# Kernel optimization log

Measured on AMD Instinct MI355X. Metric: run time of the kernel, lower is better.

## Reference

```python
import jax, jax.numpy as jnp
import numpy as np
from jax import lax

B, L_IN, DEC_LEN = 1024, 2048, 64
H = 128            # hidden_size
CARD, EMB = 200, 16  # categorical feature cardinality / embedding dim
VDIM = 4
IN_SIZE = EMB + 1 + 1  # cat-embed + continuous feat (Linear(1,1)) + target value


def setup_inputs() -> dict:
    key = jax.random.key(0)
    k = jax.random.split(key, 19)
    s = 1.0 / np.sqrt(H)  # torch LSTM/Linear default init scale
    u = lambda kk, shape: jax.random.uniform(kk, shape, minval=-s, maxval=s, dtype=jnp.float32)
    return {
        "cat_in": jax.random.randint(k[0], (B, L_IN), 0, CARD, dtype=jnp.int32),
        "cont_in": jax.random.normal(k[1], (B, L_IN, 1), dtype=jnp.float32),
        "X_in": jax.random.normal(k[2], (B, L_IN, 1), dtype=jnp.float32),
        "cat_out": jax.random.randint(k[3], (B, DEC_LEN), 0, CARD, dtype=jnp.int32),
        "cont_out": jax.random.normal(k[4], (B, DEC_LEN, 1), dtype=jnp.float32),
        # learned params
        "emb_table": jax.random.normal(k[5], (CARD, EMB), dtype=jnp.float32) * 0.02,
        "cont_w": jax.random.normal(k[6], (1, 1), dtype=jnp.float32) * 0.5,  # Linear(1,1,bias=False)
        "Wih_e": u(k[7], (4 * H, IN_SIZE)),
        "Whh_e": u(k[8], (4 * H, H)),
        "b_e": u(k[9], (4 * H,)),   # b_ih + b_hh folded together
        "Wih_d": u(k[10], (4 * H, IN_SIZE)),
        "Whh_d": u(k[11], (4 * H, H)),
        "b_d": u(k[12], (4 * H,)),
        "Wm": u(k[13], (1, H)), "bm": u(k[14], (1,)),
        "Ws": u(k[15], (1, H)), "bs": u(k[16], (1,)),
        "Wv": u(k[17], (VDIM, H)), "bv": u(k[18], (VDIM,)),
    }


def _lstm_cell(x, h, c, Wih, Whh, b):
    # torch gate order: i, f, g, o
    gates = x @ Wih.T + h @ Whh.T + b  # [B, 4H]
    i, f, g, o = jnp.split(gates, 4, axis=-1)
    c_new = jax.nn.sigmoid(f) * c + jax.nn.sigmoid(i) * jnp.tanh(g)
    h_new = jax.nn.sigmoid(o) * jnp.tanh(c_new)
    return h_new, c_new


def reference(cat_in, cont_in, X_in, cat_out, cont_out, emb_table, cont_w,
              Wih_e, Whh_e, b_e, Wih_d, Whh_d, b_d, Wm, bm, Ws, bs, Wv, bv):
    w00 = cont_w[0, 0]
    # feature embedding: Embedding for categorical, Linear(1,1,no bias) for continuous
    feats_in_embed = jnp.concatenate([emb_table[cat_in], cont_in * w00], axis=-1)  # [B,L,EMB+1]
    enc_in = jnp.concatenate([feats_in_embed, X_in], axis=-1)                      # [B,L,IN_SIZE]

    h0 = jnp.zeros((X_in.shape[0], H), dtype=X_in.dtype)

    def enc_step(carry, xt):
        h, c = carry
        return _lstm_cell(xt, h, c, Wih_e, Whh_e, b_e), None

    # encoder outputs are unused downstream; only the final (h, c) state matters
    (h, c), _ = lax.scan(enc_step, (h0, h0), jnp.swapaxes(enc_in, 0, 1))

    feats_out_embed = jnp.concatenate([emb_table[cat_out], cont_out * w00], axis=-1)  # [B,D,EMB+1]

    def dec_step(carry, feats_next):
        h, c, x_prev, f_prev = carry
        xt = jnp.concatenate([f_prev, x_prev], axis=-1)  # [B, IN_SIZE]
        h, c = _lstm_cell(xt, h, c, Wih_d, Whh_d, b_d)
        mu = h @ Wm.T + bm                     # [B,1]
        std = jax.nn.softplus(h @ Ws.T + bs)   # [B,1]
        v = h @ Wv.T + bv                      # [B,VDIM]
        return (h, c, mu, feats_next), (mu, std, v)

    init = (h, c, X_in[:, -1, :], feats_in_embed[:, -1, :])
    _, (means, stds, vs) = lax.scan(dec_step, init, jnp.swapaxes(feats_out_embed, 0, 1))
    # [D,B,*] -> [B,D,*]
    return (jnp.swapaxes(means, 0, 1), jnp.swapaxes(stds, 0, 1), jnp.swapaxes(vs, 0, 1))
```

## Files before the change

### kernel.cpp

```cpp
#include <hip/hip_runtime.h>
#include <math.h>

typedef _Float16 half8 __attribute__((ext_vector_type(8)));
typedef float float4v __attribute__((ext_vector_type(4)));

constexpr int Lc   = 2048;
constexpr int DECc = 64;
constexpr int Hc   = 128;
constexpr int EMBc = 16;
constexpr int INc  = 18;
constexpr int NBc  = 4;
constexpr int NTc  = 512;
constexpr int CARD = 200;
constexpr int ZS   = 160;


__device__ __forceinline__ float rcp_(float x) { return __builtin_amdgcn_rcpf(x); }
__device__ __forceinline__ float sigm(float x) { return rcp_(1.0f + __expf(-x)); }
__device__ __forceinline__ float tanh_(float x) { return 2.0f * rcp_(1.0f + __expf(-2.0f * x)) - 1.0f; }
__device__ __forceinline__ float softplus_(float x) { return __logf(1.0f + __expf(x)); }

__device__ __forceinline__ float sel4(float4v v, int q) {
    const float a = (q & 1) ? v[1] : v[0];
    const float b = (q & 1) ? v[3] : v[2];
    return (q & 2) ? b : a;
}

__global__ __launch_bounds__(NTc, 1) void rnnar_kernel(
    const int*   __restrict__ cat_in,  const float* __restrict__ cont_in,
    const float* __restrict__ X_in,    const int*   __restrict__ cat_out,
    const float* __restrict__ cont_out,const float* __restrict__ emb_table,
    const float* __restrict__ cont_w,
    const float* __restrict__ Wih_e, const float* __restrict__ Whh_e, const float* __restrict__ b_e,
    const float* __restrict__ Wih_d, const float* __restrict__ Whh_d, const float* __restrict__ b_d,
    const float* __restrict__ Wm, const float* __restrict__ bm,
    const float* __restrict__ Ws, const float* __restrict__ bs,
    const float* __restrict__ Wv, const float* __restrict__ bv,
    float* __restrict__ out)
{
    __shared__ _Float16      z_lds[2][NBc * ZS];
    __shared__ _Float16      emb_lds[CARD * EMBc];
    __shared__ _Float16      xo4[DECc * NBc];
    __shared__ unsigned char catob4[DECc * NBc];
    __shared__ float         h32_lds[NBc * 132];
    __shared__ float         wh_lds[6 * Hc];
    __shared__ float         hb_lds[8];
    __shared__ float         mu_lds[4];
    __shared__ float4v       x_lds[8][4][4][16];

    const int tid  = threadIdx.x;
    const int lane = tid & 63;
    const int wv   = tid >> 6;
    const int q    = lane >> 4;
    const int col  = lane & 15;
    const int cell = 16 * wv + col;
    const int bx   = col & 3;
    const int gu   = col >> 2;
    const int gb   = col & 3;
    const int b0   = blockIdx.x * NBc;
    const float w00 = cont_w[0];

    {
        int* z32 = (int*)&z_lds[0][0];
        for (int i = tid; i < NBc * ZS; i += NTc) z32[i] = 0;
    }
    for (int i = tid; i < CARD * EMBc; i += NTc) emb_lds[i] = (_Float16)emb_table[i];
    if (tid < NBc * DECc) {
        const int t = tid >> 2, b = tid & 3;
        catob4[tid] = (unsigned char)cat_out[(b0 + b) * DECc + t];
        xo4[tid]    = (_Float16)(cont_out[(b0 + b) * DECc + t] * w00);
    }
    for (int i = tid; i < 6 * Hc; i += NTc) {
        const int o = i >> 7, k = i & 127;
        wh_lds[i] = (o == 0) ? Wm[k] : (o == 1) ? Ws[k] : Wv[(o - 2) * Hc + k];
    }
    if (tid == 0) { hb_lds[0] = bm[0]; hb_lds[1] = bs[0]; }
    if (tid < 4)  { hb_lds[2 + tid] = bv[tid]; mu_lds[tid] = 0.0f; }

    half8 Bf[4][5];
    float bias_s[4];
    float w17_s[4];
    #define LOAD_T(WIH, WHH, BB)                                               \
    {                                                                          \
        _Pragma("unroll")                                                      \
        for (int gt = 0; gt < 4; ++gt) {                                       \
            const int row = gt * Hc + cell;                                    \
            _Pragma("unroll")                                                  \
            for (int kt = 0; kt < 5; ++kt) {                                   \
                half8 f;                                                       \
                _Pragma("unroll")                                              \
                for (int j = 0; j < 8; ++j) {                                  \
                    const int k = 32 * kt + 8 * q + j;                         \
                    float v = 0.0f;                                            \
                    if (k < Hc)             v = WHH[row * Hc + k];             \
                    else if (k < Hc + INc)  v = WIH[row * INc + (k - Hc)];     \
                    f[j] = (_Float16)v;                                        \
                }                                                              \
                Bf[gt][kt] = f;                                                \
            }                                                                  \
            bias_s[gt] = BB[row];                                              \
            w17_s[gt]  = WIH[row * INc + 17];                                  \
        }                                                                      \
    }

    #define BUILD_X(GCAT, GCONT, GX)                                           \
    {                                                                          \
        half8 ax;                                                              \
        _Pragma("unroll") for (int j = 0; j < 8; ++j) ax[j] = (_Float16)0.0f;  \
        if (q < 2)       ax = *(const half8*)&emb_lds[(GCAT) * EMBc + 8 * q];  \
        else if (q == 2) { ax[0] = (_Float16)((GCONT) * w00); ax[1] = (_Float16)(GX); } \
        _Pragma("unroll")                                                      \
        for (int gt = 0; gt < 4; ++gt) {                                       \
            float4v a = {bias_s[gt], bias_s[gt], bias_s[gt], bias_s[gt]};      \
            a = __builtin_amdgcn_mfma_f32_16x16x32_f16(ax, Bf[gt][4], a, 0, 0, 0); \
            x_lds[wv][q][gt][col] = a;                                         \
        }                                                                      \
    }

    LOAD_T(Wih_e, Whh_e, b_e);
    __syncthreads();

    int   g_cat;  float g_cont, g_X;
    {
        const long idx = (long)(b0 + gb) * Lc + gu;
        g_cat  = cat_in[idx];
        g_cont = cont_in[idx];
        g_X    = X_in[idx];
    }
    BUILD_X(g_cat, g_cont, g_X);

    float4v xinit[4];
    #pragma unroll
    for (int gt = 0; gt < 4; ++gt) xinit[gt] = x_lds[wv][0][gt][col];

    int p = 0;
    float c_reg = 0.f;

    for (int t = 0; t < Lc; ++t) {
        const _Float16* zr = &z_lds[p][0];
        _Float16*       zw = &z_lds[p ^ 1][0];

        const _Float16* ap = zr + bx * ZS + 8 * q;
        half8 Az[4];
        #pragma unroll
        for (int kt = 0; kt < 4; ++kt) Az[kt] = *(const half8*)(ap + 32 * kt);

        float4v acc[4];
        #pragma unroll
        for (int gt = 0; gt < 4; ++gt) {
            float4v a = xinit[gt];
            #pragma unroll
            for (int kt = 0; kt < 4; ++kt)
                a = __builtin_amdgcn_mfma_f32_16x16x32_f16(Az[kt], Bf[gt][kt], a, 0, 0, 0);
            acc[gt] = a;
        }

        if ((t & 3) == 2 && t + 2 < Lc) {
            const long idx = (long)(b0 + gb) * Lc + (t + 2 + gu);
            g_cat  = cat_in[idx];
            g_cont = cont_in[idx];
            g_X    = X_in[idx];
        }
        if ((t & 3) == 3 && t + 1 < Lc) BUILD_X(g_cat, g_cont, g_X);

        {
            const int sn = (t + 1) & 3;
            #pragma unroll
            for (int gt = 0; gt < 4; ++gt) xinit[gt] = x_lds[wv][sn][gt][col];
        }

        const float gi = sel4(acc[0], q);
        const float gf = sel4(acc[1], q);
        const float gg = sel4(acc[2], q);
        const float go = sel4(acc[3], q);

        const float cn = sigm(gf) * c_reg + sigm(gi) * tanh_(gg);
        c_reg = cn;
        zw[q * ZS + cell] = (_Float16)(sigm(go) * tanh_(cn));

        __syncthreads();
        p ^= 1;
    }

    LOAD_T(Wih_d, Whh_d, b_d);
    const float bm0 = hb_lds[0], bs0 = hb_lds[1];

    float4v acc_pre[4];
    {
        const long idx = (long)(b0 + bx) * Lc + (Lc - 1);
        const int   c0 = cat_in[idx];
        const float cc = cont_in[idx];
        const float xx = X_in[idx];
        half8 ax;
        #pragma unroll
        for (int j = 0; j < 8; ++j) ax[j] = (_Float16)0.0f;
        if (q < 2)       ax = *(const half8*)&emb_lds[c0 * EMBc + 8 * q];
        else if (q == 2) { ax[0] = (_Float16)(cc * w00); ax[1] = (_Float16)xx; }
        #pragma unroll
        for (int gt = 0; gt < 4; ++gt) {
            float4v a = {bias_s[gt], bias_s[gt], bias_s[gt], bias_s[gt]};
            acc_pre[gt] = __builtin_amdgcn_mfma_f32_16x16x32_f16(ax, Bf[gt][4], a, 0, 0, 0);
        }
    }
    __syncthreads();

    for (int t = 0; t < DECc; ++t) {
        const _Float16* zr = &z_lds[p][0];
        _Float16*       zw = &z_lds[p ^ 1][0];

        const float muq = mu_lds[q];

        const _Float16* ap = zr + bx * ZS + 8 * q;
        half8 Az[4];
        #pragma unroll
        for (int kt = 0; kt < 4; ++kt) Az[kt] = *(const half8*)(ap + 32 * kt);

        float4v acc[4];
        #pragma unroll
        for (int gt = 0; gt < 4; ++gt) {
            float4v a = acc_pre[gt];
            #pragma unroll
            for (int kt = 0; kt < 4; ++kt)
                a = __builtin_amdgcn_mfma_f32_16x16x32_f16(Az[kt], Bf[gt][kt], a, 0, 0, 0);
            acc[gt] = a;
        }

        {
            half8 ax;
            #pragma unroll
            for (int j = 0; j < 8; ++j) ax[j] = (_Float16)0.0f;
            if (q < 2)       ax = *(const half8*)&emb_lds[(int)catob4[t * 4 + bx] * EMBc + 8 * q];
            else if (q == 2) ax[0] = xo4[t * 4 + bx];
            #pragma unroll
            for (int gt = 0; gt < 4; ++gt) {
                float4v a = {bias_s[gt], bias_s[gt], bias_s[gt], bias_s[gt]};
                acc_pre[gt] = __builtin_amdgcn_mfma_f32_16x16x32_f16(ax, Bf[gt][4], a, 0, 0, 0);
            }
        }

        const float gi = sel4(acc[0], q) + muq * w17_s[0];
        const float gf = sel4(acc[1], q) + muq * w17_s[1];
        const float gg = sel4(acc[2], q) + muq * w17_s[2];
        const float go = sel4(acc[3], q) + muq * w17_s[3];

        const float cn = sigm(gf) * c_reg + sigm(gi) * tanh_(gg);
        c_reg = cn;
        const float hv = sigm(go) * tanh_(cn);
        zw[q * ZS + cell] = (_Float16)hv;
        h32_lds[q * 132 + cell] = hv;

        __syncthreads();

        if (tid < 384) {
            const int grp = tid >> 4;
            const int l16 = tid & 15;
            const int b   = grp & 3, o = grp >> 2;
            float s = 0.0f;
            #pragma unroll
            for (int j = 0; j < 8; ++j) {
                const int k = l16 + 16 * j;
                s += wh_lds[o * Hc + k] * h32_lds[b * 132 + k];
            }
            s += __shfl_xor(s, 1);
            s += __shfl_xor(s, 2);
            s += __shfl_xor(s, 4);
            s += __shfl_xor(s, 8);
            if (l16 == 0) {
                const int gb2 = b0 + b;
                if (o == 0) {
                    const float mu = s + bm0;
                    out[gb2 * DECc + t] = mu;
                    mu_lds[b] = mu;
                } else if (o == 1) {
                    out[65536 + gb2 * DECc + t] = softplus_(s + bs0);
                } else {
                    out[131072 + (gb2 * DECc + t) * 4 + (o - 2)] = s + hb_lds[2 + (o - 2)];
                }
            }
        }
        __syncthreads();
        p ^= 1;
    }
    #undef LOAD_T
    #undef BUILD_X
}

extern "C" void kernel_launch(void* const* d_in, const int* in_sizes, int n_in,
                              void* d_out, int out_size, void* d_ws, size_t ws_size,
                              hipStream_t stream) {
    rnnar_kernel<<<1024 / NBc, NTc, 0, stream>>>(
        (const int*)d_in[0],   (const float*)d_in[1],  (const float*)d_in[2],
        (const int*)d_in[3],   (const float*)d_in[4],  (const float*)d_in[5],
        (const float*)d_in[6],
        (const float*)d_in[7], (const float*)d_in[8],  (const float*)d_in[9],
        (const float*)d_in[10],(const float*)d_in[11], (const float*)d_in[12],
        (const float*)d_in[13],(const float*)d_in[14],
        (const float*)d_in[15],(const float*)d_in[16],
        (const float*)d_in[17],(const float*)d_in[18],
        (float*)d_out);
}
```

Before: 1.244 ms.

## Preload encoder input sequence into LDS and fold input MFMA into recurrence chain

```diff
diff --git a/kernel.cpp b/kernel.cpp
--- a/kernel.cpp
+++ b/kernel.cpp
@@ -40,13 +40,15 @@
 {
     __shared__ _Float16      z_lds[2][NBc * ZS];
     __shared__ _Float16      emb_lds[CARD * EMBc];
+    __shared__ _Float16      xs04[Lc * NBc];
+    __shared__ _Float16      xs14[Lc * NBc];
+    __shared__ unsigned char catb4[Lc * NBc];
     __shared__ _Float16      xo4[DECc * NBc];
     __shared__ unsigned char catob4[DECc * NBc];
     __shared__ float         h32_lds[NBc * 132];
     __shared__ float         wh_lds[6 * Hc];
     __shared__ float         hb_lds[8];
     __shared__ float         mu_lds[4];
-    __shared__ float4v       x_lds[8][4][4][16];
 
     const int tid  = threadIdx.x;
     const int lane = tid & 63;
@@ -55,8 +57,6 @@
     const int col  = lane & 15;
     const int cell = 16 * wv + col;
     const int bx   = col & 3;
-    const int gu   = col >> 2;
-    const int gb   = col & 3;
     const int b0   = blockIdx.x * NBc;
     const float w00 = cont_w[0];
 
@@ -65,6 +65,12 @@
         for (int i = tid; i < NBc * ZS; i += NTc) z32[i] = 0;
     }
     for (int i = tid; i < CARD * EMBc; i += NTc) emb_lds[i] = (_Float16)emb_table[i];
+    for (int i = tid; i < Lc * NBc; i += NTc) {
+        const int t = i >> 2, b = i & 3;
+        catb4[i] = (unsigned char)cat_in[(b0 + b) * Lc + t];
+        xs04[i]  = (_Float16)(cont_in[(b0 + b) * Lc + t] * w00);
+        xs14[i]  = (_Float16)(X_in[(b0 + b) * Lc + t]);
+    }
     if (tid < NBc * DECc) {
         const int t = tid >> 2, b = tid & 3;
         catob4[tid] = (unsigned char)cat_out[(b0 + b) * DECc + t];
@@ -103,35 +109,23 @@
         }                                                                      \
     }
 
-    #define BUILD_X(GCAT, GCONT, GX)                                           \
-    {                                                                          \
-        half8 ax;                                                              \
-        _Pragma("unroll") for (int j = 0; j < 8; ++j) ax[j] = (_Float16)0.0f;  \
-        if (q < 2)       ax = *(const half8*)&emb_lds[(GCAT) * EMBc + 8 * q];  \
-        else if (q == 2) { ax[0] = (_Float16)((GCONT) * w00); ax[1] = (_Float16)(GX); } \
-        _Pragma("unroll")                                                      \
-        for (int gt = 0; gt < 4; ++gt) {                                       \
-            float4v a = {bias_s[gt], bias_s[gt], bias_s[gt], bias_s[gt]};      \
-            a = __builtin_amdgcn_mfma_f32_16x16x32_f16(ax, Bf[gt][4], a, 0, 0, 0); \
-            x_lds[wv][q][gt][col] = a;                                         \
-        }                                                                      \
-    }
-
     LOAD_T(Wih_e, Whh_e, b_e);
+    float4v bias4[4];
+    #pragma unroll
+    for (int gt = 0; gt < 4; ++gt)
+        bias4[gt] = (float4v){bias_s[gt], bias_s[gt], bias_s[gt], bias_s[gt]};
     __syncthreads();
 
-    int   g_cat;  float g_cont, g_X;
-    {
-        const long idx = (long)(b0 + gb) * Lc + gu;
-        g_cat  = cat_in[idx];
-        g_cont = cont_in[idx];
-        g_X    = X_in[idx];
-    }
-    BUILD_X(g_cat, g_cont, g_X);
-
-    float4v xinit[4];
+    half8 ax;
     #pragma unroll
-    for (int gt = 0; gt < 4; ++gt) xinit[gt] = x_lds[wv][0][gt][col];
+    for (int j = 0; j < 8; ++j) ax[j] = (_Float16)0.0f;
+    if (q < 2) {
+        const int c4 = (int)catb4[0 * 4 + bx];
+        ax = *(const half8*)&emb_lds[c4 * EMBc + 8 * q];
+    } else if (q == 2) {
+        ax[0] = xs04[bx];
+        ax[1] = xs14[bx];
+    }
 
     int p = 0;
     float c_reg = 0.f;
@@ -148,25 +142,23 @@
         float4v acc[4];
         #pragma unroll
         for (int gt = 0; gt < 4; ++gt) {
-            float4v a = xinit[gt];
+            float4v a = __builtin_amdgcn_mfma_f32_16x16x32_f16(ax, Bf[gt][4], bias4[gt], 0, 0, 0);
             #pragma unroll
             for (int kt = 0; kt < 4; ++kt)
                 a = __builtin_amdgcn_mfma_f32_16x16x32_f16(Az[kt], Bf[gt][kt], a, 0, 0, 0);
             acc[gt] = a;
         }
 
-        if ((t & 3) == 2 && t + 2 < Lc) {
-            const long idx = (long)(b0 + gb) * Lc + (t + 2 + gu);
-            g_cat  = cat_in[idx];
-            g_cont = cont_in[idx];
-            g_X    = X_in[idx];
-        }
-        if ((t & 3) == 3 && t + 1 < Lc) BUILD_X(g_cat, g_cont, g_X);
-
-        {
-            const int sn = (t + 1) & 3;
-            #pragma unroll
-            for (int gt = 0; gt < 4; ++gt) xinit[gt] = x_lds[wv][sn][gt][col];
+        const int tn = (t + 1 < Lc) ? t + 1 : Lc - 1;
+        half8 axn;
+        #pragma unroll
+        for (int j = 0; j < 8; ++j) axn[j] = (_Float16)0.0f;
+        if (q < 2) {
+            const int c4 = (int)catb4[tn * 4 + bx];
+            axn = *(const half8*)&emb_lds[c4 * EMBc + 8 * q];
+        } else if (q == 2) {
+            axn[0] = xs04[tn * 4 + bx];
+            axn[1] = xs14[tn * 4 + bx];
         }
 
         const float gi = sel4(acc[0], q);
@@ -178,31 +170,16 @@
         c_reg = cn;
         zw[q * ZS + cell] = (_Float16)(sigm(go) * tanh_(cn));
 
+        ax = axn;
         __syncthreads();
         p ^= 1;
     }
 
     LOAD_T(Wih_d, Whh_d, b_d);
+    #pragma unroll
+    for (int gt = 0; gt < 4; ++gt)
+        bias4[gt] = (float4v){bias_s[gt], bias_s[gt], bias_s[gt], bias_s[gt]};
     const float bm0 = hb_lds[0], bs0 = hb_lds[1];
-
-    float4v acc_pre[4];
-    {
-        const long idx = (long)(b0 + bx) * Lc + (Lc - 1);
-        const int   c0 = cat_in[idx];
-        const float cc = cont_in[idx];
-        const float xx = X_in[idx];
-        half8 ax;
-        #pragma unroll
-        for (int j = 0; j < 8; ++j) ax[j] = (_Float16)0.0f;
-        if (q < 2)       ax = *(const half8*)&emb_lds[c0 * EMBc + 8 * q];
-        else if (q == 2) { ax[0] = (_Float16)(cc * w00); ax[1] = (_Float16)xx; }
-        #pragma unroll
-        for (int gt = 0; gt < 4; ++gt) {
-            float4v a = {bias_s[gt], bias_s[gt], bias_s[gt], bias_s[gt]};
-            acc_pre[gt] = __builtin_amdgcn_mfma_f32_16x16x32_f16(ax, Bf[gt][4], a, 0, 0, 0);
-        }
-    }
-    __syncthreads();
 
     for (int t = 0; t < DECc; ++t) {
         const _Float16* zr = &z_lds[p][0];
@@ -218,24 +195,21 @@
         float4v acc[4];
         #pragma unroll
         for (int gt = 0; gt < 4; ++gt) {
-            float4v a = acc_pre[gt];
+            float4v a = __builtin_amdgcn_mfma_f32_16x16x32_f16(ax, Bf[gt][4], bias4[gt], 0, 0, 0);
             #pragma unroll
             for (int kt = 0; kt < 4; ++kt)
                 a = __builtin_amdgcn_mfma_f32_16x16x32_f16(Az[kt], Bf[gt][kt], a, 0, 0, 0);
             acc[gt] = a;
         }
 
-        {
-            half8 ax;
-            #pragma unroll
-            for (int j = 0; j < 8; ++j) ax[j] = (_Float16)0.0f;
-            if (q < 2)       ax = *(const half8*)&emb_lds[(int)catob4[t * 4 + bx] * EMBc + 8 * q];
-            else if (q == 2) ax[0] = xo4[t * 4 + bx];
-            #pragma unroll
-            for (int gt = 0; gt < 4; ++gt) {
-                float4v a = {bias_s[gt], bias_s[gt], bias_s[gt], bias_s[gt]};
-                acc_pre[gt] = __builtin_amdgcn_mfma_f32_16x16x32_f16(ax, Bf[gt][4], a, 0, 0, 0);
-            }
+        half8 axn;
+        #pragma unroll
+        for (int j = 0; j < 8; ++j) axn[j] = (_Float16)0.0f;
+        if (q < 2) {
+            const int c4 = (int)catob4[t * 4 + bx];
+            axn = *(const half8*)&emb_lds[c4 * EMBc + 8 * q];
+        } else if (q == 2) {
+            axn[0] = xo4[t * 4 + bx];
         }
 
         const float gi = sel4(acc[0], q) + muq * w17_s[0];
@@ -249,6 +223,7 @@
         zw[q * ZS + cell] = (_Float16)hv;
         h32_lds[q * 132 + cell] = hv;
 
+        ax = axn;
         __syncthreads();
 
         if (tid < 384) {
@@ -282,7 +257,6 @@
         p ^= 1;
     }
     #undef LOAD_T
-    #undef BUILD_X
 }
 
 extern "C" void kernel_launch(void* const* d_in, const int* in_sizes, int n_in,
```

Measured after the change: 1.401 ms. 1.13x slower.
